# Kernel tuning notes

Hardware: AMD Instinct MI355X
Metric: run time of the kernel (lower is better)

Reference implementation:

```python
import jax, jax.numpy as jnp
import numpy as np

H = 256  # LSTM hidden units per layer

def _cell(xt, h, c, W, U, b):
    # Keras LSTMCell: gate order i, f, g(cell), o; sigmoid recurrent activation, tanh activation
    z = xt @ W + h @ U + b  # (B, 4H)
    i, f, g, o = jnp.split(z, 4, axis=-1)
    c_new = jax.nn.sigmoid(f) * c + jax.nn.sigmoid(i) * jnp.tanh(g)
    h_new = jax.nn.sigmoid(o) * jnp.tanh(c_new)
    return h_new, c_new

def _stacked_lstm(x, W1, U1, b1, W2, U2, b2):
    # x: (B, T, F). Returns concat of FINAL CELL STATES of both layers: (B, 2H)
    # (original code takes outputs[i+1][1], i.e. the c state of each LSTMCell)
    B = x.shape[0]
    def step(carry, xt):
        h1, c1, h2, c2 = carry
        h1, c1 = _cell(xt, h1, c1, W1, U1, b1)
        h2, c2 = _cell(h1, h2, c2, W2, U2, b2)
        return (h1, c1, h2, c2), None
    z0 = jnp.zeros((B, H), x.dtype)
    (h1, c1, h2, c2), _ = jax.lax.scan(step, (z0, z0, z0, z0), jnp.swapaxes(x, 0, 1))
    return jnp.concatenate([c1, c2], axis=-1)

def _glorot(key, shape):
    lim = np.sqrt(6.0 / (shape[0] + shape[1]))
    return jax.random.uniform(key, shape, jnp.float32, -lim, lim)

def _lstm_bias():
    # Keras unit_forget_bias=True: forget-gate bias initialized to 1
    return jnp.zeros((4 * H,), jnp.float32).at[H:2 * H].set(1.0)

def setup_inputs():
    key = jax.random.key(0)
    ks = jax.random.split(key, 16)
    B, T, F, ZD = 16384, 20, 80, 32
    inp = {
        "x": jax.random.normal(ks[0], (B, T, F), jnp.float32),
        "eps1": jax.random.normal(ks[1], (B, ZD), jnp.float32),
        "eps2": jax.random.normal(ks[2], (B, ZD), jnp.float32),
        # z2 stacked LSTM (input F)
        "z2_W1": _glorot(ks[3], (F, 4 * H)), "z2_U1": _glorot(ks[4], (H, 4 * H)), "z2_b1": _lstm_bias(),
        "z2_W2": _glorot(ks[5], (H, 4 * H)), "z2_U2": _glorot(ks[6], (H, 4 * H)), "z2_b2": _lstm_bias(),
        # z1 stacked LSTM (input F + z2_dim)
        "z1_W1": _glorot(ks[7], (F + ZD, 4 * H)), "z1_U1": _glorot(ks[8], (H, 4 * H)), "z1_b1": _lstm_bias(),
        "z1_W2": _glorot(ks[9], (H, 4 * H)), "z1_U2": _glorot(ks[10], (H, 4 * H)), "z1_b2": _lstm_bias(),
        # dense heads (input 2H -> ZD), linear (mu_nl=logvar_nl=None)
        "mu2_W": _glorot(ks[11], (2 * H, ZD)), "mu2_b": jnp.zeros((ZD,), jnp.float32),
        "lv2_W": _glorot(ks[12], (2 * H, ZD)), "lv2_b": jnp.zeros((ZD,), jnp.float32),
        "mu1_W": _glorot(ks[13], (2 * H, ZD)), "mu1_b": jnp.zeros((ZD,), jnp.float32),
        "lv1_W": _glorot(ks[14], (2 * H, ZD)), "lv1_b": jnp.zeros((ZD,), jnp.float32),
    }
    return inp

def reference(x, eps1, eps2,
              z2_W1, z2_U1, z2_b1, z2_W2, z2_U2, z2_b2,
              z1_W1, z1_U1, z1_b1, z1_W2, z1_U2, z1_b2,
              mu2_W, mu2_b, lv2_W, lv2_b, mu1_W, mu1_b, lv1_W, lv1_b):
    B, T, _ = x.shape
    # z2 branch
    z2_pre = _stacked_lstm(x, z2_W1, z2_U1, z2_b1, z2_W2, z2_U2, z2_b2)  # (B, 2H)
    z2_mu = z2_pre @ mu2_W + mu2_b
    z2_logvar = z2_pre @ lv2_W + lv2_b
    z2_sample = eps2 * jnp.exp(0.5 * z2_logvar) + z2_mu  # reparameterize
    # z1 branch: tile z2_sample over time, concat with x
    z2_tiled = jnp.broadcast_to(z2_sample[:, None, :], (B, T, z2_sample.shape[-1]))
    x_z2 = jnp.concatenate([x, z2_tiled], axis=-1)  # (B, T, F+ZD)
    z1_pre = _stacked_lstm(x_z2, z1_W1, z1_U1, z1_b1, z1_W2, z1_U2, z1_b2)
    z1_mu = z1_pre @ mu1_W + mu1_b
    z1_logvar = z1_pre @ lv1_W + lv1_b
    z1_sample = eps1 * jnp.exp(0.5 * z1_logvar) + z1_mu
    return (z1_mu, z1_logvar, z1_sample, z2_mu, z2_logvar, z2_sample)
```

## Files before the change

### kernel.cpp

```cpp
#include <hip/hip_runtime.h>
#include <hip/hip_bf16.h>

#define B_SZ 16384
#define T_SZ 20

typedef __attribute__((ext_vector_type(8))) __bf16 bf16x8;
typedef __attribute__((ext_vector_type(4))) float f32x4;

__device__ __forceinline__ float sigm(float x){ return 1.f/(1.f+__expf(-x)); }
__device__ __forceinline__ float tanh_(float x){ return 1.f-2.f/(__expf(2.f*x)+1.f); }

#define OFF_L1Z2 0
#define OFF_L2Z2 360448
#define OFF_L1Z1 884736
#define OFF_L2Z1 1277952
#define OFF_HZ2  1802240
#define OFF_HZ1  1835008
#define WP_TOT   1867776

__global__ void prep_w(const float* __restrict__ W0, const float* __restrict__ U0,
                       const float* __restrict__ W1, const float* __restrict__ U1,
                       const float* __restrict__ W2, const float* __restrict__ U2,
                       const float* __restrict__ W3, const float* __restrict__ U3,
                       const float* __restrict__ muW2, const float* __restrict__ lvW2,
                       const float* __restrict__ muW1, const float* __restrict__ lvW1,
                       __bf16* __restrict__ wp)
{
    int idx = blockIdx.x * 256 + threadIdx.x;
    if (idx >= WP_TOT) return;
    if (idx < OFF_HZ2) {
        const float *W, *U;
        int Fx, Kx, KT, local;
        if (idx < OFF_L2Z2)      { W = W0; U = U0; Fx = 80;  Kx = 96;  KT = 11; local = idx; }
        else if (idx < OFF_L1Z1) { W = W1; U = U1; Fx = 256; Kx = 256; KT = 16; local = idx - OFF_L2Z2; }
        else if (idx < OFF_L2Z1) { W = W2; U = U2; Fx = 112; Kx = 128; KT = 12; local = idx - OFF_L1Z1; }
        else                     { W = W3; U = U3; Fx = 256; Kx = 256; KT = 16; local = idx - OFF_L2Z1; }
        int jj = local & 7, lane = (local >> 3) & 63, nt8 = (local >> 9) & 7, rest = local >> 12;
        int kt = rest % KT, wgn = rest / KT;
        int gate = nt8 >> 1, hh = nt8 & 1;
        int n = gate * 256 + wgn * 32 + hh * 16 + (lane & 15);
        int k = kt * 32 + ((lane >> 4) << 3) + jj;
        float v = (k < Fx) ? W[k * 1024 + n] : (k < Kx ? 0.f : U[(k - Kx) * 1024 + n]);
        wp[idx] = (__bf16)v;
    } else {
        int base = (idx < OFF_HZ1) ? OFF_HZ2 : OFF_HZ1;
        const float* mw = (idx < OFF_HZ1) ? muW2 : muW1;
        const float* lw = (idx < OFF_HZ1) ? lvW2 : lvW1;
        int local = idx - base;
        int jj = local & 7, lane = (local >> 3) & 63, nt = (local >> 9) & 3, kt = local >> 11;
        int k = kt * 32 + ((lane >> 4) << 3) + jj;
        int c16 = lane & 15;
        float v = (nt < 2) ? mw[k * 32 + nt * 16 + c16] : lw[k * 32 + (nt - 2) * 16 + c16];
        wp[idx] = (__bf16)v;
    }
}

__global__ void xconv(const float* __restrict__ x, __bf16* __restrict__ xb)
{
    int idx = blockIdx.x * 256 + threadIdx.x;
    int c8 = idx & 15, row = idx >> 4;
    bf16x8 r;
    if (c8 < 10) {
        const float4* p = reinterpret_cast<const float4*>(x + (size_t)row * 80 + c8 * 8);
        float4 u0 = p[0], u1 = p[1];
        r[0]=(__bf16)u0.x; r[1]=(__bf16)u0.y; r[2]=(__bf16)u0.z; r[3]=(__bf16)u0.w;
        r[4]=(__bf16)u1.x; r[5]=(__bf16)u1.y; r[6]=(__bf16)u1.z; r[7]=(__bf16)u1.w;
    } else {
#pragma unroll
        for (int i = 0; i < 8; ++i) r[i] = (__bf16)0.f;
    }
    *reinterpret_cast<bf16x8*>(xb + (size_t)row * 128 + c8 * 8) = r;
}

__global__ void bcast_z2(const __bf16* __restrict__ z2sb, __bf16* __restrict__ xb)
{
    int idx = blockIdx.x * 256 + threadIdx.x;
    int g = idx & 3, b = idx >> 2;
    bf16x8 v = *reinterpret_cast<const bf16x8*>(z2sb + (size_t)b * 32 + g * 8);
#pragma unroll
    for (int t = 0; t < T_SZ; ++t)
        *reinterpret_cast<bf16x8*>(xb + ((size_t)b * T_SZ + t) * 128 + 80 + g * 8) = v;
}

__device__ __forceinline__ void stage16(const __bf16* g, __bf16* l)
{
    __builtin_amdgcn_global_load_lds(
        (const __attribute__((address_space(1))) unsigned*)g,
        (__attribute__((address_space(3))) unsigned*)l, 16, 0, 0);
}

template <int KT, int KTP, int XKT, int TWOH, int FIRST>
__global__ void __launch_bounds__(256, 4)
step_gemm(const __bf16* __restrict__ xb, int t,
          const __bf16* __restrict__ hA, const __bf16* __restrict__ hB,
          const __bf16* __restrict__ wpm, const float* __restrict__ bias,
          float* __restrict__ cbuf, __bf16* __restrict__ hout)
{
    __shared__ __align__(16) __bf16 Bs[4][4096];

    const int tid = threadIdx.x;
    const int w = tid >> 6, lane = tid & 63;
    const int r16 = lane & 15, kq = lane >> 4;
    const int mid = blockIdx.x & 127, wgn = blockIdx.x >> 7;
    const int rb = mid * 128 + w * 32;
    const __bf16* wpB = wpm + (size_t)wgn * KTP * 4096;

    const __bf16 *x0 = nullptr, *x1 = nullptr;
    if (XKT > 0) {
        x0 = xb + ((size_t)(rb + r16) * T_SZ + t) * 128 + kq * 8;
        x1 = xb + ((size_t)(rb + 16 + r16) * T_SZ + t) * 128 + kq * 8;
    }
    const __bf16* hA0 = hA + (size_t)(rb + r16) * 256 + kq * 8;
    const __bf16* hA1 = hA + (size_t)(rb + 16 + r16) * 256 + kq * 8;
    const __bf16 *hB0 = nullptr, *hB1 = nullptr;
    if (TWOH) {
        hB0 = hB + (size_t)(rb + r16) * 256 + kq * 8;
        hB1 = hB + (size_t)(rb + 16 + r16) * 256 + kq * 8;
    }

    f32x4 acc[8][2];
#pragma unroll
    for (int nt = 0; nt < 8; ++nt)
#pragma unroll
        for (int m = 0; m < 2; ++m) acc[nt][m] = f32x4{0.f, 0.f, 0.f, 0.f};

    bf16x8 aR[3][2];

    auto ap = [&](int kt, int m) -> const __bf16* {
        if (XKT > 0 && kt < XKT) return (m ? x1 : x0) + kt * 32;
        int kk = kt - XKT;
        if (!TWOH || kk < 8) return (m ? hA1 : hA0) + kk * 32;
        return (m ? hB1 : hB0) + (kk - 8) * 32;
    };

#define STG(K) { const __bf16* g_ = wpB + (size_t)(K) * 4096 + tid * 8;            \
                 stage16(g_, &Bs[(K) & 3][tid * 8]);                               \
                 stage16(g_ + 2048, &Bs[(K) & 3][2048 + tid * 8]); }
#define LDA(K) { aR[(K) % 3][0] = *reinterpret_cast<const bf16x8*>(ap((K), 0));    \
                 aR[(K) % 3][1] = *reinterpret_cast<const bf16x8*>(ap((K), 1)); }
#define CMP(K) { const __bf16* bp_ = &Bs[(K) & 3][lane * 8];                       \
    _Pragma("unroll") for (int nt = 0; nt < 8; ++nt) {                             \
        bf16x8 bv_ = *reinterpret_cast<const bf16x8*>(bp_ + nt * 512);             \
        acc[nt][0] = __builtin_amdgcn_mfma_f32_16x16x32_bf16(aR[(K)%3][0], bv_, acc[nt][0], 0, 0, 0); \
        acc[nt][1] = __builtin_amdgcn_mfma_f32_16x16x32_bf16(aR[(K)%3][1], bv_, acc[nt][1], 0, 0, 0); } }
#define PH(K) if constexpr ((K) < KT) {                                            \
    __builtin_amdgcn_sched_barrier(0);                                             \
    if constexpr ((K) + 2 < KT) { STG((K) + 2); LDA((K) + 2); }                    \
    { constexpr int cnt_ = 4 * (((K) + 1 < KT) ? 1 : 0) + 4 * (((K) + 2 < KT) ? 1 : 0); \
      asm volatile("s_waitcnt vmcnt(%0)" :: "n"(cnt_) : "memory"); }               \
    __builtin_amdgcn_s_barrier();                                                  \
    __builtin_amdgcn_sched_barrier(0);                                             \
    CMP(K); }

    STG(0); LDA(0);
    if constexpr (KT > 1) { STG(1); LDA(1); }

    PH(0)  PH(1)  PH(2)  PH(3)  PH(4)  PH(5)  PH(6)  PH(7)
    PH(8)  PH(9)  PH(10) PH(11) PH(12) PH(13) PH(14) PH(15)

#undef STG
#undef LDA
#undef CMP
#undef PH

    float bg[2][4];
#pragma unroll
    for (int hh = 0; hh < 2; ++hh)
#pragma unroll
        for (int gate = 0; gate < 4; ++gate)
            bg[hh][gate] = bias[gate * 256 + wgn * 32 + hh * 16 + r16];

#pragma unroll
    for (int m = 0; m < 2; ++m)
#pragma unroll
        for (int hh = 0; hh < 2; ++hh) {
            const int hcol = wgn * 32 + hh * 16 + r16;
            f32x4 zi = acc[0 + hh][m], zf = acc[2 + hh][m], zg = acc[4 + hh][m], zo = acc[6 + hh][m];
#pragma unroll
            for (int q = 0; q < 4; ++q) {
                int row = rb + m * 16 + kq * 4 + q;
                size_t off = (size_t)row * 256 + hcol;
                float cn;
                if (FIRST) {
                    cn = sigm(zi[q] + bg[hh][0]) * tanh_(zg[q] + bg[hh][2]);
                } else {
                    float co = cbuf[off];
                    cn = sigm(zf[q] + bg[hh][1]) * co
                       + sigm(zi[q] + bg[hh][0]) * tanh_(zg[q] + bg[hh][2]);
                }
                cbuf[off] = cn;
                hout[off] = (__bf16)(sigm(zo[q] + bg[hh][3]) * tanh_(cn));
            }
        }
}

__global__ void __launch_bounds__(128, 4)
head_mfma(const float* __restrict__ c1, const float* __restrict__ c2,
          const __bf16* __restrict__ hp, const float* __restrict__ mub,
          const float* __restrict__ lvb, const float* __restrict__ eps,
          float* __restrict__ omu, float* __restrict__ olv, float* __restrict__ osm,
          __bf16* __restrict__ osb)
{
    const int tid = threadIdx.x;
    const int w = tid >> 6, lane = tid & 63;
    const int r16 = lane & 15, kq = lane >> 4;
    const int rb = blockIdx.x * 64 + w * 32;

    f32x4 acc[4][2];
#pragma unroll
    for (int nt = 0; nt < 4; ++nt)
#pragma unroll
        for (int m = 0; m < 2; ++m) acc[nt][m] = f32x4{0.f, 0.f, 0.f, 0.f};

#pragma unroll
    for (int kt = 0; kt < 16; ++kt) {
        const float* cs = (kt < 8) ? c1 : c2;
        int k = (kt & 7) * 32 + kq * 8;
        bf16x8 a[2];
#pragma unroll
        for (int m = 0; m < 2; ++m) {
            const float* pr = cs + (size_t)(rb + m * 16 + r16) * 256 + k;
            float4 u0 = reinterpret_cast<const float4*>(pr)[0];
            float4 u1 = reinterpret_cast<const float4*>(pr)[1];
            a[m][0]=(__bf16)u0.x; a[m][1]=(__bf16)u0.y; a[m][2]=(__bf16)u0.z; a[m][3]=(__bf16)u0.w;
            a[m][4]=(__bf16)u1.x; a[m][5]=(__bf16)u1.y; a[m][6]=(__bf16)u1.z; a[m][7]=(__bf16)u1.w;
        }
        const __bf16* hb = hp + kt * 2048 + lane * 8;
#pragma unroll
        for (int nt = 0; nt < 4; ++nt) {
            bf16x8 bv = *reinterpret_cast<const bf16x8*>(hb + nt * 512);
            acc[nt][0] = __builtin_amdgcn_mfma_f32_16x16x32_bf16(a[0], bv, acc[nt][0], 0, 0, 0);
            acc[nt][1] = __builtin_amdgcn_mfma_f32_16x16x32_bf16(a[1], bv, acc[nt][1], 0, 0, 0);
        }
    }

#pragma unroll
    for (int m = 0; m < 2; ++m)
#pragma unroll
        for (int q = 0; q < 4; ++q) {
            int row = rb + m * 16 + kq * 4 + q;
#pragma unroll
            for (int z = 0; z < 2; ++z) {
                int zc = z * 16 + r16;
                float mu = acc[z][m][q] + mub[zc];
                float lv = acc[z + 2][m][q] + lvb[zc];
                int idx = row * 32 + zc;
                omu[idx] = mu;
                olv[idx] = lv;
                float s = fmaf(eps[idx], expf(0.5f * lv), mu);
                osm[idx] = s;
                if (osb) osb[idx] = (__bf16)s;
            }
        }
}

extern "C" void kernel_launch(void* const* d_in, const int* in_sizes, int n_in,
                              void* d_out, int out_size, void* d_ws, size_t ws_size,
                              hipStream_t stream)
{
    const float* x    = (const float*)d_in[0];
    const float* eps1 = (const float*)d_in[1];
    const float* eps2 = (const float*)d_in[2];
    const float* z2W1 = (const float*)d_in[3];
    const float* z2U1 = (const float*)d_in[4];
    const float* z2b1 = (const float*)d_in[5];
    const float* z2W2 = (const float*)d_in[6];
    const float* z2U2 = (const float*)d_in[7];
    const float* z2b2 = (const float*)d_in[8];
    const float* z1W1 = (const float*)d_in[9];
    const float* z1U1 = (const float*)d_in[10];
    const float* z1b1 = (const float*)d_in[11];
    const float* z1W2 = (const float*)d_in[12];
    const float* z1U2 = (const float*)d_in[13];
    const float* z1b2 = (const float*)d_in[14];
    const float* mu2W = (const float*)d_in[15];
    const float* mu2b = (const float*)d_in[16];
    const float* lv2W = (const float*)d_in[17];
    const float* lv2b = (const float*)d_in[18];
    const float* mu1W = (const float*)d_in[19];
    const float* mu1b = (const float*)d_in[20];
    const float* lv1W = (const float*)d_in[21];
    const float* lv1b = (const float*)d_in[22];

    char* ws = (char*)d_ws;
    __bf16* wp   = (__bf16*)ws;
    __bf16* z2sb = (__bf16*)(ws + 4194304);
    __bf16* xb   = (__bf16*)(ws + 5242880);
    __bf16* h1a  = (__bf16*)(ws + 89128960);
    __bf16* h2a  = (__bf16*)(ws + 97517568);
    __bf16* h1b  = (__bf16*)(ws + 105906176);
    __bf16* h2b  = (__bf16*)(ws + 114294784);
    float*  c1   = (float*)(ws + 122683392);
    float*  c2   = (float*)(ws + 139460608);

    __bf16* h1[2] = {h1a, h1b};
    __bf16* h2[2] = {h2a, h2b};

    float* out = (float*)d_out;
    const int BZ = B_SZ * 32;
    float* z1mu = out;           float* z1lv = out + BZ;     float* z1sm = out + 2 * BZ;
    float* z2mu = out + 3 * BZ;  float* z2lv = out + 4 * BZ; float* z2sm = out + 5 * BZ;

    xconv<<<B_SZ * T_SZ * 16 / 256, 256, 0, stream>>>(x, xb);
    prep_w<<<7296, 256, 0, stream>>>(z2W1, z2U1, z2W2, z2U2, z1W1, z1U1, z1W2, z1U2,
                                     mu2W, lv2W, mu1W, lv1W, wp);

    step_gemm<3, 11, 3, 0, 1><<<1024, 256, 0, stream>>>(xb, 0, h1a, nullptr,
                                                        wp + OFF_L1Z2, z2b1, c1, h1[0]);
    step_gemm<8, 16, 0, 1, 1><<<1024, 256, 0, stream>>>(xb, 0, h1[0], h2a,
                                                        wp + OFF_L2Z2, z2b2, c2, h2[0]);
    for (int t = 1; t < T_SZ; ++t) {
        int cur = t & 1, prv = cur ^ 1;
        step_gemm<11, 11, 3, 0, 0><<<1024, 256, 0, stream>>>(xb, t, h1[prv], nullptr,
                                                             wp + OFF_L1Z2, z2b1, c1, h1[cur]);
        step_gemm<16, 16, 0, 1, 0><<<1024, 256, 0, stream>>>(xb, t, h1[cur], h2[prv],
                                                             wp + OFF_L2Z2, z2b2, c2, h2[cur]);
    }
    head_mfma<<<256, 128, 0, stream>>>(c1, c2, wp + OFF_HZ2, mu2b, lv2b, eps2,
                                       z2mu, z2lv, z2sm, z2sb);
    bcast_z2<<<B_SZ * 4 / 256, 256, 0, stream>>>(z2sb, xb);

    step_gemm<4, 12, 4, 0, 1><<<1024, 256, 0, stream>>>(xb, 0, h1a, nullptr,
                                                        wp + OFF_L1Z1, z1b1, c1, h1[0]);
    step_gemm<8, 16, 0, 1, 1><<<1024, 256, 0, stream>>>(xb, 0, h1[0], h2a,
                                                        wp + OFF_L2Z1, z1b2, c2, h2[0]);
    for (int t = 1; t < T_SZ; ++t) {
        int cur = t & 1, prv = cur ^ 1;
        step_gemm<12, 12, 4, 0, 0><<<1024, 256, 0, stream>>>(xb, t, h1[prv], nullptr,
                                                             wp + OFF_L1Z1, z1b1, c1, h1[cur]);
        step_gemm<16, 16, 0, 1, 0><<<1024, 256, 0, stream>>>(xb, t, h1[cur], h2[prv],
                                                             wp + OFF_L2Z1, z1b2, c2, h2[cur]);
    }
    head_mfma<<<256, 128, 0, stream>>>(c1, c2, wp + OFF_HZ1, mu1b, lv1b, eps1,
                                       z1mu, z1lv, z1sm, nullptr);
}
```

Baseline: 2.223 ms.

## Retile LSTM step GEMM to 256x256 tiles staging activations in LDS

The per-timestep gate GEMM moves from 128-row x 128-column tiles (1024 blocks of 256 threads, weights staged in LDS) to 256-row x 256-column tiles (256 blocks of 512 threads). Activations are now staged in LDS through global_load_lds and shared by all waves, while each wave keeps its weight fragments in registers. The packed weight layout in prep_w changes to match the 64-hidden-column slices. The aim is to cut redundant global and L2 traffic for activations and weights and raise MFMA work per load. In exchange, only 256 blocks launch, which may underfill the GPU, and each thread holds 32 accumulators, raising register pressure.

```diff
diff --git a/kernel.cpp b/kernel.cpp
--- a/kernel.cpp
+++ b/kernel.cpp
@@ -35,10 +35,10 @@
         else if (idx < OFF_L1Z1) { W = W1; U = U1; Fx = 256; Kx = 256; KT = 16; local = idx - OFF_L2Z2; }
         else if (idx < OFF_L2Z1) { W = W2; U = U2; Fx = 112; Kx = 128; KT = 12; local = idx - OFF_L1Z1; }
         else                     { W = W3; U = U3; Fx = 256; Kx = 256; KT = 16; local = idx - OFF_L2Z1; }
-        int jj = local & 7, lane = (local >> 3) & 63, nt8 = (local >> 9) & 7, rest = local >> 12;
+        int jj = local & 7, lane = (local >> 3) & 63, nt16 = (local >> 9) & 15, rest = local >> 13;
         int kt = rest % KT, wgn = rest / KT;
-        int gate = nt8 >> 1, hh = nt8 & 1;
-        int n = gate * 256 + wgn * 32 + hh * 16 + (lane & 15);
+        int gate = nt16 & 3, hh = nt16 >> 2;
+        int n = gate * 256 + wgn * 64 + hh * 16 + (lane & 15);
         int k = kt * 32 + ((lane >> 4) << 3) + jj;
         float v = (k < Fx) ? W[k * 1024 + n] : (k < Kx ? 0.f : U[(k - Kx) * 1024 + n]);
         wp[idx] = (__bf16)v;
@@ -90,108 +90,100 @@
 }
 
 template <int KT, int KTP, int XKT, int TWOH, int FIRST>
-__global__ void __launch_bounds__(256, 4)
+__global__ void __launch_bounds__(512, 2)
 step_gemm(const __bf16* __restrict__ xb, int t,
           const __bf16* __restrict__ hA, const __bf16* __restrict__ hB,
           const __bf16* __restrict__ wpm, const float* __restrict__ bias,
           float* __restrict__ cbuf, __bf16* __restrict__ hout)
 {
-    __shared__ __align__(16) __bf16 Bs[4][4096];
+    __shared__ __align__(16) __bf16 As[3][8192];
 
     const int tid = threadIdx.x;
     const int w = tid >> 6, lane = tid & 63;
     const int r16 = lane & 15, kq = lane >> 4;
-    const int mid = blockIdx.x & 127, wgn = blockIdx.x >> 7;
-    const int rb = mid * 128 + w * 32;
-    const __bf16* wpB = wpm + (size_t)wgn * KTP * 4096;
-
-    const __bf16 *x0 = nullptr, *x1 = nullptr;
-    if (XKT > 0) {
-        x0 = xb + ((size_t)(rb + r16) * T_SZ + t) * 128 + kq * 8;
-        x1 = xb + ((size_t)(rb + 16 + r16) * T_SZ + t) * 128 + kq * 8;
-    }
-    const __bf16* hA0 = hA + (size_t)(rb + r16) * 256 + kq * 8;
-    const __bf16* hA1 = hA + (size_t)(rb + 16 + r16) * 256 + kq * 8;
-    const __bf16 *hB0 = nullptr, *hB1 = nullptr;
-    if (TWOH) {
-        hB0 = hB + (size_t)(rb + r16) * 256 + kq * 8;
-        hB1 = hB + (size_t)(rb + 16 + r16) * 256 + kq * 8;
-    }
-
-    f32x4 acc[8][2];
-#pragma unroll
-    for (int nt = 0; nt < 8; ++nt)
-#pragma unroll
-        for (int m = 0; m < 2; ++m) acc[nt][m] = f32x4{0.f, 0.f, 0.f, 0.f};
-
-    bf16x8 aR[3][2];
-
-    auto ap = [&](int kt, int m) -> const __bf16* {
-        if (XKT > 0 && kt < XKT) return (m ? x1 : x0) + kt * 32;
-        int kk = kt - XKT;
-        if (!TWOH || kk < 8) return (m ? hA1 : hA0) + kk * 32;
-        return (m ? hB1 : hB0) + (kk - 8) * 32;
-    };
-
-#define STG(K) { const __bf16* g_ = wpB + (size_t)(K) * 4096 + tid * 8;            \
-                 stage16(g_, &Bs[(K) & 3][tid * 8]);                               \
-                 stage16(g_ + 2048, &Bs[(K) & 3][2048 + tid * 8]); }
-#define LDA(K) { aR[(K) % 3][0] = *reinterpret_cast<const bf16x8*>(ap((K), 0));    \
-                 aR[(K) % 3][1] = *reinterpret_cast<const bf16x8*>(ap((K), 1)); }
-#define CMP(K) { const __bf16* bp_ = &Bs[(K) & 3][lane * 8];                       \
-    _Pragma("unroll") for (int nt = 0; nt < 8; ++nt) {                             \
-        bf16x8 bv_ = *reinterpret_cast<const bf16x8*>(bp_ + nt * 512);             \
-        acc[nt][0] = __builtin_amdgcn_mfma_f32_16x16x32_bf16(aR[(K)%3][0], bv_, acc[nt][0], 0, 0, 0); \
-        acc[nt][1] = __builtin_amdgcn_mfma_f32_16x16x32_bf16(aR[(K)%3][1], bv_, acc[nt][1], 0, 0, 0); } }
-#define PH(K) if constexpr ((K) < KT) {                                            \
-    __builtin_amdgcn_sched_barrier(0);                                             \
-    if constexpr ((K) + 2 < KT) { STG((K) + 2); LDA((K) + 2); }                    \
-    { constexpr int cnt_ = 4 * (((K) + 1 < KT) ? 1 : 0) + 4 * (((K) + 2 < KT) ? 1 : 0); \
-      asm volatile("s_waitcnt vmcnt(%0)" :: "n"(cnt_) : "memory"); }               \
-    __builtin_amdgcn_s_barrier();                                                  \
-    __builtin_amdgcn_sched_barrier(0);                                             \
+    const int wr = w >> 2, wc = w & 3;
+    const int mid = blockIdx.x & 63, wgn = blockIdx.x >> 6;
+    const int rb = mid * 256;
+    const __bf16* wpB = wpm + (size_t)wgn * KTP * 8192;
+    const __bf16* pBW = wpB + wc * 2048 + lane * 8;
+
+    const int srow0 = rb + w * 32 + (lane >> 2);
+    const int ksub  = (lane & 3) * 8;
+    const __bf16* pA0 = hA + (size_t)srow0 * 256 + ksub;
+    const __bf16* pA1 = hA + (size_t)(srow0 + 16) * 256 + ksub;
+    const __bf16* px0 = (XKT > 0) ? xb + ((size_t)srow0 * T_SZ + t) * 128 + ksub : pA0;
+    const __bf16* px1 = (XKT > 0) ? xb + ((size_t)(srow0 + 16) * T_SZ + t) * 128 + ksub : pA1;
+    const __bf16* pH0 = TWOH ? hB + (size_t)srow0 * 256 + ksub : pA0;
+    const __bf16* pH1 = TWOH ? hB + (size_t)(srow0 + 16) * 256 + ksub : pA1;
+
+    f32x4 acc[4][8];
+#pragma unroll
+    for (int g = 0; g < 4; ++g)
+#pragma unroll
+        for (int m = 0; m < 8; ++m) acc[g][m] = f32x4{0.f, 0.f, 0.f, 0.f};
+
+    bf16x8 bR[3][4];
+
+#define ASRC(K, P0, PA, PH_) \
+    ((K) < XKT ? (P0) + (K) * 32 \
+               : ((!TWOH || ((K) - XKT) < 8) ? (PA) + ((K) - XKT) * 32 \
+                                             : (PH_) + ((K) - XKT - 8) * 32))
+#define STG_A(K) { stage16(ASRC(K, px0, pA0, pH0), &As[(K) % 3][w * 1024]); \
+                   stage16(ASRC(K, px1, pA1, pH1), &As[(K) % 3][w * 1024 + 512]); }
+#define LDB(K) { _Pragma("unroll") for (int nt = 0; nt < 4; ++nt) \
+                   bR[(K) % 3][nt] = *reinterpret_cast<const bf16x8*>(pBW + (size_t)(K) * 8192 + nt * 512); }
+#define CMP(K) { const __bf16* ab_ = &As[(K) % 3][(wr * 128 + r16) * 32 + kq * 8]; \
+    bf16x8 a_[8]; \
+    _Pragma("unroll") for (int m = 0; m < 8; ++m) \
+        a_[m] = *reinterpret_cast<const bf16x8*>(ab_ + m * 512); \
+    _Pragma("unroll") for (int m = 0; m < 8; ++m) \
+        _Pragma("unroll") for (int g = 0; g < 4; ++g) \
+            acc[g][m] = __builtin_amdgcn_mfma_f32_16x16x32_bf16(a_[m], bR[(K) % 3][g], acc[g][m], 0, 0, 0); }
+#define PH(K) if constexpr ((K) < KT) { \
+    __builtin_amdgcn_sched_barrier(0); \
+    if constexpr ((K) + 1 < KT) STG_A((K) + 1); \
+    if constexpr ((K) + 2 < KT) LDB((K) + 2); \
+    { constexpr int c_ = 2 * (((K) + 1 < KT) ? 1 : 0) + 4 * (((K) + 2 < KT) ? 1 : 0); \
+      asm volatile("s_waitcnt vmcnt(%0)" :: "n"(c_) : "memory"); } \
+    __builtin_amdgcn_s_barrier(); \
+    __builtin_amdgcn_sched_barrier(0); \
     CMP(K); }
 
-    STG(0); LDA(0);
-    if constexpr (KT > 1) { STG(1); LDA(1); }
+    STG_A(0); LDB(0);
+    if constexpr (KT > 1) LDB(1);
 
     PH(0)  PH(1)  PH(2)  PH(3)  PH(4)  PH(5)  PH(6)  PH(7)
     PH(8)  PH(9)  PH(10) PH(11) PH(12) PH(13) PH(14) PH(15)
 
-#undef STG
-#undef LDA
+#undef ASRC
+#undef STG_A
+#undef LDB
 #undef CMP
 #undef PH
 
-    float bg[2][4];
-#pragma unroll
-    for (int hh = 0; hh < 2; ++hh)
-#pragma unroll
-        for (int gate = 0; gate < 4; ++gate)
-            bg[hh][gate] = bias[gate * 256 + wgn * 32 + hh * 16 + r16];
-
-#pragma unroll
-    for (int m = 0; m < 2; ++m)
-#pragma unroll
-        for (int hh = 0; hh < 2; ++hh) {
-            const int hcol = wgn * 32 + hh * 16 + r16;
-            f32x4 zi = acc[0 + hh][m], zf = acc[2 + hh][m], zg = acc[4 + hh][m], zo = acc[6 + hh][m];
-#pragma unroll
-            for (int q = 0; q < 4; ++q) {
-                int row = rb + m * 16 + kq * 4 + q;
-                size_t off = (size_t)row * 256 + hcol;
-                float cn;
-                if (FIRST) {
-                    cn = sigm(zi[q] + bg[hh][0]) * tanh_(zg[q] + bg[hh][2]);
-                } else {
-                    float co = cbuf[off];
-                    cn = sigm(zf[q] + bg[hh][1]) * co
-                       + sigm(zi[q] + bg[hh][0]) * tanh_(zg[q] + bg[hh][2]);
-                }
-                cbuf[off] = cn;
-                hout[off] = (__bf16)(sigm(zo[q] + bg[hh][3]) * tanh_(cn));
+    const int hcol = wgn * 64 + wc * 16 + r16;
+    float bg[4];
+#pragma unroll
+    for (int g = 0; g < 4; ++g) bg[g] = bias[g * 256 + hcol];
+
+#pragma unroll
+    for (int m = 0; m < 8; ++m) {
+        f32x4 zi = acc[0][m], zf = acc[1][m], zg = acc[2][m], zo = acc[3][m];
+#pragma unroll
+        for (int q = 0; q < 4; ++q) {
+            int row = rb + wr * 128 + m * 16 + kq * 4 + q;
+            size_t off = (size_t)row * 256 + hcol;
+            float cn;
+            if (FIRST) {
+                cn = sigm(zi[q] + bg[0]) * tanh_(zg[q] + bg[2]);
+            } else {
+                float co = cbuf[off];
+                cn = sigm(zf[q] + bg[1]) * co + sigm(zi[q] + bg[0]) * tanh_(zg[q] + bg[2]);
             }
+            cbuf[off] = cn;
+            hout[off] = (__bf16)(sigm(zo[q] + bg[3]) * tanh_(cn));
         }
+    }
 }
 
 __global__ void __launch_bounds__(128, 4)
@@ -305,31 +297,31 @@
     prep_w<<<7296, 256, 0, stream>>>(z2W1, z2U1, z2W2, z2U2, z1W1, z1U1, z1W2, z1U2,
                                      mu2W, lv2W, mu1W, lv1W, wp);
 
-    step_gemm<3, 11, 3, 0, 1><<<1024, 256, 0, stream>>>(xb, 0, h1a, nullptr,
-                                                        wp + OFF_L1Z2, z2b1, c1, h1[0]);
-    step_gemm<8, 16, 0, 1, 1><<<1024, 256, 0, stream>>>(xb, 0, h1[0], h2a,
-                                                        wp + OFF_L2Z2, z2b2, c2, h2[0]);
+    step_gemm<3, 11, 3, 0, 1><<<256, 512, 0, stream>>>(xb, 0, h1a, nullptr,
+                                                       wp + OFF_L1Z2, z2b1, c1, h1[0]);
+    step_gemm<8, 16, 0, 1, 1><<<256, 512, 0, stream>>>(xb, 0, h1[0], h2a,
+                                                       wp + OFF_L2Z2, z2b2, c2, h2[0]);
     for (int t = 1; t < T_SZ; ++t) {
         int cur = t & 1, prv = cur ^ 1;
-        step_gemm<11, 11, 3, 0, 0><<<1024, 256, 0, stream>>>(xb, t, h1[prv], nullptr,
-                                                             wp + OFF_L1Z2, z2b1, c1, h1[cur]);
-        step_gemm<16, 16, 0, 1, 0><<<1024, 256, 0, stream>>>(xb, t, h1[cur], h2[prv],
-                                                             wp + OFF_L2Z2, z2b2, c2, h2[cur]);
+        step_gemm<11, 11, 3, 0, 0><<<256, 512, 0, stream>>>(xb, t, h1[prv], nullptr,
+                                                            wp + OFF_L1Z2, z2b1, c1, h1[cur]);
+        step_gemm<16, 16, 0, 1, 0><<<256, 512, 0, stream>>>(xb, t, h1[cur], h2[prv],
+                                                            wp + OFF_L2Z2, z2b2, c2, h2[cur]);
     }
     head_mfma<<<256, 128, 0, stream>>>(c1, c2, wp + OFF_HZ2, mu2b, lv2b, eps2,
                                        z2mu, z2lv, z2sm, z2sb);
     bcast_z2<<<B_SZ * 4 / 256, 256, 0, stream>>>(z2sb, xb);
 
-    step_gemm<4, 12, 4, 0, 1><<<1024, 256, 0, stream>>>(xb, 0, h1a, nullptr,
-                                                        wp + OFF_L1Z1, z1b1, c1, h1[0]);
-    step_gemm<8, 16, 0, 1, 1><<<1024, 256, 0, stream>>>(xb, 0, h1[0], h2a,
-                                                        wp + OFF_L2Z1, z1b2, c2, h2[0]);
+    step_gemm<4, 12, 4, 0, 1><<<256, 512, 0, stream>>>(xb, 0, h1a, nullptr,
+                                                       wp + OFF_L1Z1, z1b1, c1, h1[0]);
+    step_gemm<8, 16, 0, 1, 1><<<256, 512, 0, stream>>>(xb, 0, h1[0], h2a,
+                                                       wp + OFF_L2Z1, z1b2, c2, h2[0]);
     for (int t = 1; t < T_SZ; ++t) {
         int cur = t & 1, prv = cur ^ 1;
-        step_gemm<12, 12, 4, 0, 0><<<1024, 256, 0, stream>>>(xb, t, h1[prv], nullptr,
-                                                             wp + OFF_L1Z1, z1b1, c1, h1[cur]);
-        step_gemm<16, 16, 0, 1, 0><<<1024, 256, 0, stream>>>(xb, t, h1[cur], h2[prv],
-                                                             wp + OFF_L2Z1, z1b2, c2, h2[cur]);
+        step_gemm<12, 12, 4, 0, 0><<<256, 512, 0, stream>>>(xb, t, h1[prv], nullptr,
+                                                            wp + OFF_L1Z1, z1b1, c1, h1[cur]);
+        step_gemm<16, 16, 0, 1, 0><<<256, 512, 0, stream>>>(xb, t, h1[cur], h2[prv],
+                                                            wp + OFF_L2Z1, z1b2, c2, h2[cur]);
     }
     head_mfma<<<256, 128, 0, stream>>>(c1, c2, wp + OFF_HZ1, mu1b, lv1b, eps1,
                                        z1mu, z1lv, z1sm, nullptr);
```

Result: faster. 2.144 ms (-3.5%).
